# Performance work log

Hardware: AMD Instinct MI355X
Metric: run time of the kernel (lower is better)

The kernel has to match this reference:

```python
import jax, jax.numpy as jnp
import numpy as np

B = 8
C = 128          # channels
H = 1024         # sparse (hidden) channels in bottleneck
START = 128      # start_frames
SPARSE = 8192    # sparse_frames
K = 512          # k_sparse
N_UP = 6         # log2(SPARSE/START) upsample blocks
EPS = 1e-5


def conv1d(x, w, b, stride=1, pad=0):
    # x: (B, Cin, L), w: (Cout, Cin, K)
    y = jax.lax.conv_general_dilated(
        x, w, window_strides=(stride,), padding=[(pad, pad)],
        dimension_numbers=('NCW', 'OIW', 'NCW'))
    return y + b[None, :, None]


def batch_norm(x, g, beta):
    # training-mode BatchNorm1d: stats over (batch, length) per channel
    m = x.mean(axis=(0, 2), keepdims=True)
    v = x.var(axis=(0, 2), keepdims=True)
    return (x - m) * jax.lax.rsqrt(v + EPS) * g[None, :, None] + beta[None, :, None]


def lrelu(x):
    return jnp.where(x >= 0, x, 0.2 * x)


def setup_inputs() -> dict:
    key = jax.random.key(0)
    ks = jax.random.split(key, 16)
    s = 0.05
    return {
        'x': jax.random.normal(ks[0], (B, C, START), dtype=jnp.float32),
        'up_w': jax.random.normal(ks[1], (N_UP, C, C, 3), dtype=jnp.float32) * s,
        'up_b': jnp.zeros((N_UP, C), dtype=jnp.float32),
        'up_g': jnp.ones((N_UP, C), dtype=jnp.float32),
        'up_beta': jnp.zeros((N_UP, C), dtype=jnp.float32),
        'up_out_w': jax.random.normal(ks[2], (C, C, 3), dtype=jnp.float32) * s,
        'up_out_b': jnp.zeros((C,), dtype=jnp.float32),
        # SparseBottleneck 1x1 convs (stored as (out,in) matrices)
        'sb_up_w': jax.random.normal(ks[3], (H, C), dtype=jnp.float32) * s,
        'sb_up_b': jnp.zeros((H,), dtype=jnp.float32),
        'sal_w': jax.random.normal(ks[4], (H, C), dtype=jnp.float32) * s,
        'sal_b': jnp.zeros((H,), dtype=jnp.float32),
        'sb_down_w': jax.random.normal(ks[5], (C, H), dtype=jnp.float32) * s,
        'sb_down_b': jnp.zeros((C,), dtype=jnp.float32),
        'dn_w': jax.random.normal(ks[6], (3, C, C, 7), dtype=jnp.float32) * s,
        'dn_b': jnp.zeros((3, C), dtype=jnp.float32),
        'dn_g': jnp.ones((3, C), dtype=jnp.float32),
        'dn_beta': jnp.zeros((3, C), dtype=jnp.float32),
    }


def reference(x, up_w, up_b, up_g, up_beta, up_out_w, up_out_b,
              sb_up_w, sb_up_b, sal_w, sal_b, sb_down_w, sb_down_b,
              dn_w, dn_b, dn_g, dn_beta):
    # ---- ConvUpsample: 128 -> 8192 frames ----
    for i in range(N_UP):
        x = jnp.repeat(x, 2, axis=-1)
        x = conv1d(x, up_w[i], up_b[i], stride=1, pad=1)
        x = lrelu(batch_norm(x, up_g[i], up_beta[i]))
    x = conv1d(x, up_out_w, up_out_b, stride=1, pad=1)  # (B, C, 8192)

    # ---- SparseBottleneck ----
    sig = jnp.einsum('bcl,hc->bhl', x, sb_up_w) + sb_up_b[None, :, None]   # (B,H,L)
    sal = jnp.einsum('bcl,hc->bhl', x, sal_w) + sal_b[None, :, None]       # (B,H,L)
    flat = jax.nn.softmax(sal.reshape(B, -1), axis=-1)   # softmax over H*L
    vals, idx = jax.lax.top_k(flat, K)                   # (B, K)
    sparse = jnp.zeros_like(flat).at[jnp.arange(B)[:, None], idx].set(vals)
    sal = sparse.reshape(sal.shape)
    x = sig * sal                                         # gated, (B,H,L)
    x = jnp.einsum('bhl,ch->bcl', x, sb_down_w) + sb_down_b[None, :, None]

    # ---- down stack: 8192 -> 128 frames ----
    for i in range(3):
        x = conv1d(x, dn_w[i], dn_b[i], stride=4, pad=3)
        x = lrelu(x)
        x = batch_norm(x, dn_g[i], dn_beta[i])
    return x  # (B, C, 128)
```

## Files before the change

kernel.cpp:

```cpp
#include <hip/hip_runtime.h>
#include <hip/hip_bf16.h>


#define DEV_INLINE __device__ __forceinline__

constexpr int NB   = 8;
constexpr int NC   = 128;
constexpr int NH   = 1024;
constexpr int LFULL= 8192;
constexpr int KSEL = 512;
constexpr int CAP  = 32768;

typedef __attribute__((ext_vector_type(4))) float f32x4;
typedef __attribute__((ext_vector_type(8))) short bf16x8;

DEV_INLINE unsigned monoKey(float f) {
    unsigned u = __float_as_uint(f);
    return (u & 0x80000000u) ? ~u : (u | 0x80000000u);
}
DEV_INLINE float keyToF(unsigned k) {
    unsigned u = (k & 0x80000000u) ? (k ^ 0x80000000u) : ~k;
    return __uint_as_float(u);
}
DEV_INLINE unsigned monoKey16(unsigned u) {
    return (u & 0x8000u) ? ((~u) & 0xFFFFu) : (u | 0x8000u);
}
DEV_INLINE unsigned bf16r(float f) {
    unsigned u = __float_as_uint(f);
    return (u + 0x7FFFu + ((u >> 16) & 1u)) >> 16;
}
DEV_INLINE float lrelu(float v) { return v >= 0.f ? v : 0.2f * v; }
DEV_INLINE float f4c(const float4& v, int k) {
    return k == 0 ? v.x : k == 1 ? v.y : k == 2 ? v.z : v.w;
}
DEV_INLINE int swz4(int p) { return p ^ ((p >> 3) & 7); }

DEV_INLINE void loadg4(const float* __restrict__ rowp, int g0, int L, float* e) {
    if (g0 >= 0 && g0 + 4 <= L) {
        float4 v = *(const float4*)(rowp + g0);
        e[0] = v.x; e[1] = v.y; e[2] = v.z; e[3] = v.w;
    } else {
#pragma unroll
        for (int t = 0; t < 4; t++) {
            int g = g0 + t;
            e[t] = (g >= 0 && g < L) ? rowp[g] : 0.f;
        }
    }
}

__global__ __launch_bounds__(256) void prep_k(
    const float* __restrict__ up_w, const float* __restrict__ up_out_w,
    const float* __restrict__ dn_w, float* __restrict__ wprep)
{
    int idx = blockIdx.x * 256 + threadIdx.x;
    if (idx < 393216) {
        int layer = idx >> 16;
        int r0 = idx & 65535;
        int c = r0 >> 9, r = (r0 >> 7) & 3, o = r0 & 127;
        const float* wsrc = up_w + ((size_t)layer * 128 + o) * 384 + c * 3;
        float w0 = wsrc[0], w1 = wsrc[1], w2 = wsrc[2];
        wprep[idx] = (r == 0) ? w0 : (r == 1) ? (w1 + w2) : (r == 2) ? (w0 + w1) : w2;
    } else if (idx < 442368) {
        int r0 = idx - 393216;
        int c = r0 / 384, k = (r0 / 128) % 3, o = r0 & 127;
        wprep[idx] = up_out_w[((size_t)o * 128 + c) * 3 + k];
    } else {
        int r0 = idx - 442368;
        int layer = r0 / 114688;
        int r1 = r0 - layer * 114688;
        int c = r1 / 896, k = (r1 / 128) % 7, o = r1 & 127;
        wprep[idx] = dn_w[((size_t)layer * 128 + o) * 896 + c * 7 + k];
    }
}

__global__ __launch_bounds__(256) void prepA_k(
    const float* __restrict__ up_w, const float* __restrict__ up_out_w,
    unsigned short* __restrict__ afrag)
{
    int idx = blockIdx.x * 256 + threadIdx.x;
    if (idx >= 221184) return;
    int rid = idx >> 6, lane = idx & 63;
    const int r15 = lane & 15, g = lane >> 4;
    unsigned short vals[8];
    if (rid < 3072) {
        int L  = rid >> 9;
        int r0 = rid & 511;
        int f = r0 & 3, ks = (r0 >> 2) & 1, cc = (r0 >> 3) & 1;
        int wo = (r0 >> 4) & 1, half = (r0 >> 5) & 1, ptap = (r0 >> 6) & 3;
        int o = wo * 64 + f * 16 + r15;
        int cb = cc * 64 + ks * 32 + g * 8;
#pragma unroll
        for (int e = 0; e < 8; e++) {
            const float* ws = up_w + (((size_t)L * 128 + o) * 128 + (cb + e)) * 3;
            float w0 = ws[0], w1 = ws[1], w2 = ws[2];
            float v = (ptap == 0) ? w0 : (ptap == 1) ? (w1 + w2)
                    : (ptap == 2) ? (w0 + w1) : w2;
            unsigned hi = bf16r(v);
            if (half == 0) vals[e] = (unsigned short)hi;
            else vals[e] = (unsigned short)bf16r(v - __uint_as_float(hi << 16));
        }
    } else {
        int r2 = rid - 3072;
        int f = r2 & 3, ks = (r2 >> 2) & 1, cc = (r2 >> 3) & 1;
        int wo = (r2 >> 4) & 1, half = (r2 >> 5) & 1, tap = r2 >> 6;
        int o = wo * 64 + f * 16 + r15;
        int cb = cc * 64 + ks * 32 + g * 8;
#pragma unroll
        for (int e = 0; e < 8; e++) {
            float v = up_out_w[((size_t)o * 128 + (cb + e)) * 3 + tap];
            unsigned hi = bf16r(v);
            if (half == 0) vals[e] = (unsigned short)hi;
            else vals[e] = (unsigned short)bf16r(v - __uint_as_float(hi << 16));
        }
    }
    unsigned pk[4];
#pragma unroll
    for (int q = 0; q < 4; q++)
        pk[q] = (unsigned)vals[2*q] | ((unsigned)vals[2*q+1] << 16);
    *(uint4*)(afrag + (size_t)rid * 512 + lane * 8) = make_uint4(pk[0], pk[1], pk[2], pk[3]);
}

__global__ __launch_bounds__(256) void redstats_k(
    const float* __restrict__ partial, int nb, float* __restrict__ stats)
{
    const int c = threadIdx.x;
    float s0 = 0.f, s1 = 0.f, s2 = 0.f, s3 = 0.f;
    for (int i = blockIdx.x * 4; i < nb; i += gridDim.x * 4) {
        s0 += partial[(size_t)(i + 0) * 256 + c];
        s1 += partial[(size_t)(i + 1) * 256 + c];
        s2 += partial[(size_t)(i + 2) * 256 + c];
        s3 += partial[(size_t)(i + 3) * 256 + c];
    }
    float s = (s0 + s1) + (s2 + s3);
    if (s != 0.f || blockIdx.x == 0) atomicAdd(&stats[c], s);
}

template<int INMODE>
__global__ __launch_bounds__(512) void mconvU_k(
    const float* __restrict__ in, float* __restrict__ out,
    const unsigned short* __restrict__ afrag, const float* __restrict__ bias,
    const float* __restrict__ stp, const float* __restrict__ gp,
    const float* __restrict__ btp, float inv_n,
    float* __restrict__ partial, int L_in)
{
    __shared__ unsigned short Xh[66 * 64], Xl[66 * 64];
    __shared__ float scs[NC], shs[NC];
    __shared__ float sstat[256];

    const int b = blockIdx.y, tile0 = blockIdx.x * 64, tid = threadIdx.x;
    const int lane = tid & 63, wid = tid >> 6;
    const int wo = wid >> 2, par = (wid >> 1) & 1, jh = wid & 1;
    const int r15 = lane & 15, g = lane >> 4;
    const int bid = b * gridDim.x + blockIdx.x;

    if (tid < 256) sstat[tid] = 0.f;
    if (INMODE > 0) {
        for (int c = tid; c < NC; c += 512) {
            float m  = stp[c] * inv_n;
            float va = stp[NC + c] * inv_n - m * m;
            float sc = gp[c] * rsqrtf(va + 1e-5f);
            scs[c] = sc;
            shs[c] = btp[c] - m * sc;
        }
    }

    f32x4 acc[4][2];
#pragma unroll
    for (int i = 0; i < 4; i++)
#pragma unroll
        for (int j = 0; j < 2; j++) acc[i][j] = (f32x4)(0.f);

    for (int cc = 0; cc < 2; cc++) {
        __syncthreads();
        {
            int r = tid & 63;
            int l = tile0 - 1 + r;
            for (int c0 = (tid >> 6); c0 < 64; c0 += 8) {
                int c = cc * 64 + c0;
                float v = 0.f;
                if (l >= 0 && l < L_in) {
                    v = in[((size_t)b * NC + c) * L_in + l];
                    if (INMODE > 0) v = lrelu(v * scs[c] + shs[c]);
                }
                unsigned hi = bf16r(v);
                unsigned lo = bf16r(v - __uint_as_float(hi << 16));
                unsigned bo = ((unsigned)(r * 128 + c0 * 2)) ^ (((unsigned)(r & 7)) << 4);
                *(unsigned short*)((char*)Xh + bo) = (unsigned short)hi;
                *(unsigned short*)((char*)Xl + bo) = (unsigned short)lo;
            }
            if (tid < 128) {
                int r2 = 64 + (tid >> 6);
                int l2 = tile0 - 1 + r2;
                int c0 = tid & 63;
                int c = cc * 64 + c0;
                float v = 0.f;
                if (l2 >= 0 && l2 < L_in) {
                    v = in[((size_t)b * NC + c) * L_in + l2];
                    if (INMODE > 0) v = lrelu(v * scs[c] + shs[c]);
                }
                unsigned hi = bf16r(v);
                unsigned lo = bf16r(v - __uint_as_float(hi << 16));
                unsigned bo = ((unsigned)(r2 * 128 + c0 * 2)) ^ (((unsigned)(r2 & 7)) << 4);
                *(unsigned short*)((char*)Xh + bo) = (unsigned short)hi;
                *(unsigned short*)((char*)Xl + bo) = (unsigned short)lo;
            }
        }
        __syncthreads();
#pragma unroll
        for (int pt = 0; pt < 2; pt++) {
            const int ptap = par * 2 + pt;
            const int roff = (ptap == 0) ? 0 : (ptap == 3) ? 2 : 1;
#pragma unroll
            for (int combo = 0; combo < 3; combo++) {
                const int ah = (combo == 2) ? 1 : 0;
                const unsigned short* Xs = (combo == 1) ? Xl : Xh;
                bf16x8 af[8];
#pragma unroll
                for (int ks = 0; ks < 2; ks++)
#pragma unroll
                    for (int f = 0; f < 4; f++) {
                        int rec = ((((ptap * 2 + ah) * 2 + wo) * 2 + cc) * 2 + ks) * 4 + f;
                        af[ks * 4 + f] = *(const bf16x8*)(afrag + (size_t)rec * 512 + lane * 8);
                    }
#pragma unroll
                for (int ks = 0; ks < 2; ks++) {
                    bf16x8 bf_[2];
#pragma unroll
                    for (int j = 0; j < 2; j++) {
                        int row = (jh * 2 + j) * 16 + r15 + roff;
                        unsigned bo = ((unsigned)(row * 128 + ks * 64 + g * 16))
                                    ^ (((unsigned)(row & 7)) << 4);
                        bf_[j] = *(const bf16x8*)((const char*)Xs + bo);
                    }
#pragma unroll
                    for (int i = 0; i < 4; i++)
#pragma unroll
                        for (int j = 0; j < 2; j++)
                            acc[i][j] = __builtin_amdgcn_mfma_f32_16x16x32_bf16(
                                af[ks * 4 + i], bf_[j], acc[i][j], 0, 0, 0);
                }
            }
        }
    }

    const int L_out = 2 * L_in;
#pragma unroll
    for (int i = 0; i < 4; i++) {
#pragma unroll
        for (int r = 0; r < 4; r++) {
            const int o = wo * 64 + i * 16 + g * 4 + r;
            const float bv = bias[o];
            float s1 = 0.f, s2 = 0.f;
#pragma unroll
            for (int j = 0; j < 2; j++) {
                float v = acc[i][j][r] + bv;
                int lout = 2 * (tile0 + (jh * 2 + j) * 16 + r15) + par;
                out[((size_t)b * NC + o) * L_out + lout] = v;
                s1 += v; s2 += v * v;
            }
#pragma unroll
            for (int m = 1; m < 16; m <<= 1) {
                s1 += __shfl_xor(s1, m);
                s2 += __shfl_xor(s2, m);
            }
            if (r15 == 0) {
                atomicAdd(&sstat[o], s1);
                atomicAdd(&sstat[NC + o], s2);
            }
        }
    }
    __syncthreads();
    if (tid < 256) partial[(size_t)bid * 256 + tid] = sstat[tid];
}

__global__ __launch_bounds__(512) void mconvF_k(
    const float* __restrict__ in, float* __restrict__ out,
    const unsigned short* __restrict__ afrag, const float* __restrict__ bias,
    const float* __restrict__ stp, const float* __restrict__ gp,
    const float* __restrict__ btp, float inv_n,
    unsigned short* __restrict__ xtout)
{
    __shared__ unsigned short Xh[130 * 64], Xl[130 * 64];
    __shared__ float scs[NC], shs[NC];

    const int b = blockIdx.y, l0 = blockIdx.x * 128, tid = threadIdx.x;
    const int lane = tid & 63, wid = tid >> 6;
    const int wo = wid >> 2, wl = (wid & 3) * 32;
    const int r15 = lane & 15, g = lane >> 4;

    for (int c = tid; c < NC; c += 512) {
        float m  = stp[c] * inv_n;
        float va = stp[NC + c] * inv_n - m * m;
        float sc = gp[c] * rsqrtf(va + 1e-5f);
        scs[c] = sc;
        shs[c] = btp[c] - m * sc;
    }

    f32x4 acc[4][2];
#pragma unroll
    for (int i = 0; i < 4; i++)
#pragma unroll
        for (int j = 0; j < 2; j++) acc[i][j] = (f32x4)(0.f);

    for (int cc = 0; cc < 2; cc++) {
        __syncthreads();
        {
            int r = tid & 127;
            int l = l0 - 1 + r;
            for (int c0 = (tid >> 7); c0 < 64; c0 += 4) {
                int c = cc * 64 + c0;
                float v = 0.f;
                if (l >= 0 && l < LFULL) {
                    v = in[((size_t)b * NC + c) * LFULL + l];
                    v = lrelu(v * scs[c] + shs[c]);
                }
                unsigned hi = bf16r(v);
                unsigned lo = bf16r(v - __uint_as_float(hi << 16));
                unsigned bo = ((unsigned)(r * 128 + c0 * 2)) ^ (((unsigned)(r & 7)) << 4);
                *(unsigned short*)((char*)Xh + bo) = (unsigned short)hi;
                *(unsigned short*)((char*)Xl + bo) = (unsigned short)lo;
            }
            if (tid < 128) {
                int r2 = 128 + (tid >> 6);
                int l2 = l0 - 1 + r2;
                int c0 = tid & 63;
                int c = cc * 64 + c0;
                float v = 0.f;
                if (l2 >= 0 && l2 < LFULL) {
                    v = in[((size_t)b * NC + c) * LFULL + l2];
                    v = lrelu(v * scs[c] + shs[c]);
                }
                unsigned hi = bf16r(v);
                unsigned lo = bf16r(v - __uint_as_float(hi << 16));
                unsigned bo = ((unsigned)(r2 * 128 + c0 * 2)) ^ (((unsigned)(r2 & 7)) << 4);
                *(unsigned short*)((char*)Xh + bo) = (unsigned short)hi;
                *(unsigned short*)((char*)Xl + bo) = (unsigned short)lo;
            }
        }
        __syncthreads();
#pragma unroll
        for (int tap = 0; tap < 3; tap++) {
#pragma unroll
            for (int combo = 0; combo < 3; combo++) {
                const int ah = (combo == 2) ? 1 : 0;
                const unsigned short* Xs = (combo == 1) ? Xl : Xh;
                bf16x8 af[8];
#pragma unroll
                for (int ks = 0; ks < 2; ks++)
#pragma unroll
                    for (int f = 0; f < 4; f++) {
                        int rec = 3072 + ((((tap * 2 + ah) * 2 + wo) * 2 + cc) * 2 + ks) * 4 + f;
                        af[ks * 4 + f] = *(const bf16x8*)(afrag + (size_t)rec * 512 + lane * 8);
                    }
#pragma unroll
                for (int ks = 0; ks < 2; ks++) {
                    bf16x8 bf_[2];
#pragma unroll
                    for (int j = 0; j < 2; j++) {
                        int row = wl + j * 16 + r15 + tap;
                        unsigned bo = ((unsigned)(row * 128 + ks * 64 + g * 16))
                                    ^ (((unsigned)(row & 7)) << 4);
                        bf_[j] = *(const bf16x8*)((const char*)Xs + bo);
                    }
#pragma unroll
                    for (int i = 0; i < 4; i++)
#pragma unroll
                        for (int j = 0; j < 2; j++)
                            acc[i][j] = __builtin_amdgcn_mfma_f32_16x16x32_bf16(
                                af[ks * 4 + i], bf_[j], acc[i][j], 0, 0, 0);
                }
            }
        }
    }

#pragma unroll
    for (int i = 0; i < 4; i++) {
#pragma unroll
        for (int r = 0; r < 4; r++) {
            const int o = wo * 64 + i * 16 + g * 4 + r;
            const float bv = bias[o];
#pragma unroll
            for (int j = 0; j < 2; j++) {
                float v = acc[i][j][r] + bv;
                int l = l0 + wl + j * 16 + r15;
                out[((size_t)b * NC + o) * LFULL + l] = v;
                xtout[((size_t)b * LFULL + l) * NC + o] = (unsigned short)bf16r(v);
            }
        }
    }
}

template<int KW, int STRIDE, int PAD, bool UPS, int INMODE, bool OUTACT, bool STATS, int TT, bool XPOSE, int OCW>
__global__ __launch_bounds__(256) void conv7_k(
    const float* __restrict__ in, float* __restrict__ out,
    const float* __restrict__ wp, const float* __restrict__ bias,
    const float* __restrict__ stp, const float* __restrict__ gp,
    const float* __restrict__ btp, float inv_n,
    float* __restrict__ stats, unsigned short* __restrict__ xtout,
    int L_in, int L_out)
{
    constexpr int CC    = (KW == 7) ? 8 : 16;
    constexpr int PT    = 64 * TT;
    constexpr int TTO   = UPS ? 2 * TT : TT;
    constexpr int NWR   = UPS ? 4 : KW;
    constexpr int OCB   = 4 * OCW;
    constexpr int SPAN  = UPS ? (PT + 2) : ((PT - 1) * STRIDE + KW);
    constexpr int NCH   = (SPAN + 3) / 4;
    constexpr int NCH8  = (NCH + 7) & ~7;
    constexpr int XROW  = 4 * NCH8 + 4;
    constexpr int NLD   = (CC * NCH + 255) / 256;
    constexpr int XSPAN = UPS ? (TT + 2) : ((TT - 1) * STRIDE + KW);
    constexpr int STEP  = UPS ? TT : TT * STRIDE;
    constexpr int NWQ   = CC * NWR * (OCB / 4);
    static_assert((STEP & 3) == 0, "conv7 swizzle path requires STEP%4==0");
    static_assert(OCW == 4 || OCW == 8, "OCW must be 4 or 8");

    __shared__ float xs[CC][XROW];
    __shared__ float wls[CC * NWR * OCB];
    __shared__ float scs[NC], shs[NC];

    const int b = blockIdx.z, ocb = blockIdx.y, tid = threadIdx.x;
    const int t0 = blockIdx.x * PT, lane = tid & 63;
    const int wid = tid >> 6;
    const int oc0 = ocb * OCB + wid * OCW;
    const int gb = UPS ? (t0 - 1) : (t0 * STRIDE - PAD);

    if (INMODE > 0) {
        for (int c = tid; c < NC; c += 256) {
            float m  = stp[c] * inv_n;
            float va = stp[NC + c] * inv_n - m * m;
            float sc = gp[c] * rsqrtf(va + 1e-5f);
            scs[c] = sc;
            shs[c] = btp[c] - m * sc;
        }
        __syncthreads();
    }

    float acc[OCW][TTO];
#pragma unroll
    for (int i = 0; i < OCW; i++)
#pragma unroll
        for (int j = 0; j < TTO; j++) acc[i][j] = 0.f;

    float pre[NLD][4];

#define C7_STAGEW(CCBASE) do {                                              \
    for (int _u = tid; _u < NWQ; _u += 256) {                               \
        int _row = _u / (OCB / 4), _g8 = _u % (OCB / 4);                    \
        int _cl = _row / NWR, _t = _row % NWR;                              \
        ((float4*)wls)[_u] = *(const float4*)(wp +                          \
            ((size_t)((CCBASE) + _cl) * NWR + _t) * 128 + ocb * OCB + _g8 * 4); \
    }                                                                       \
} while (0)

#define C7_COMPCI(CI) do {                                                  \
    float _q[XSPAN];                                                        \
    const int _qb4 = lane * (STEP / 4);                                     \
    _Pragma("unroll")                                                       \
    for (int _u = 0; _u < XSPAN / 4; _u++) {                                \
        float4 _v = *(const float4*)&xs[CI][4 * swz4(_qb4 + _u)];           \
        _q[4*_u] = _v.x; _q[4*_u+1] = _v.y;                                 \
        _q[4*_u+2] = _v.z; _q[4*_u+3] = _v.w;                               \
    }                                                                       \
    if constexpr ((XSPAN & 3) != 0) {                                       \
        const int _pt = swz4(_qb4 + XSPAN / 4);                             \
        if constexpr ((XSPAN & 3) >= 2) {                                   \
            float2 _v = *(const float2*)&xs[CI][4 * _pt];                   \
            _q[(XSPAN & ~3)] = _v.x; _q[(XSPAN & ~3) + 1] = _v.y;           \
        }                                                                   \
        if constexpr ((XSPAN & 3) == 1)                                     \
            _q[XSPAN - 1] = xs[CI][4 * _pt];                                \
        else if constexpr ((XSPAN & 3) == 3)                                \
            _q[XSPAN - 1] = xs[CI][4 * _pt + 2];                            \
    }                                                                       \
    {                                                                       \
        _Pragma("unroll")                                                   \
        for (int _k = 0; _k < KW; _k++) {                                   \
            if constexpr (OCW == 8) {                                       \
                const float4 _w0 = *(const float4*)&wls[((CI) * NWR + _k) * OCB + wid * 8];     \
                const float4 _w1 = *(const float4*)&wls[((CI) * NWR + _k) * OCB + wid * 8 + 4]; \
                _Pragma("unroll")                                           \
                for (int _i = 0; _i < 8; _i++) {                            \
                    float _wv = f4c(_i < 4 ? _w0 : _w1, _i & 3);            \
                    _Pragma("unroll")                                       \
                    for (int _j = 0; _j < TT; _j++)                         \
                        acc[_i][_j] = fmaf(_wv, _q[_j * STRIDE + _k], acc[_i][_j]); \
                }                                                           \
            } else {                                                        \
                const float4 _w0 = *(const float4*)&wls[((CI) * NWR + _k) * OCB + wid * 4];     \
                _Pragma("unroll")                                           \
                for (int _i = 0; _i < 4; _i++) {                            \
                    float _wv = f4c(_w0, _i);                               \
                    _Pragma("unroll")                                       \
                    for (int _j = 0; _j < TT; _j++)                         \
                        acc[_i][_j] = fmaf(_wv, _q[_j * STRIDE + _k], acc[_i][_j]); \
                }                                                           \
            }                                                               \
        }                                                                   \
    }                                                                       \
} while (0)

#pragma unroll
    for (int u = 0; u < NLD; u++) {
        int idx = tid + u * 256;
        if (idx < CC * NCH) {
            int cl = idx / NCH, q = idx - cl * NCH;
            loadg4(in + ((size_t)b * NC + cl) * L_in, gb + 4 * q, L_in, pre[u]);
        }
    }
#pragma unroll
    for (int u = 0; u < NLD; u++) {
        int idx = tid + u * 256;
        if (idx < CC * NCH) {
            int cl = idx / NCH, q = idx - cl * NCH;
            int g0 = gb + 4 * q;
            float e[4];
#pragma unroll
            for (int t = 0; t < 4; t++) {
                float v = pre[u][t];
                if (INMODE > 0) {
                    int gg = g0 + t;
                    if (gg >= 0 && gg < L_in) {
                        float s = v * scs[cl] + shs[cl];
                        v = (INMODE == 2) ? lrelu(s) : s;
                    }
                }
                e[t] = v;
            }
            *(float4*)&xs[cl][4 * swz4(q)] = make_float4(e[0], e[1], e[2], e[3]);
        }
    }
    C7_STAGEW(0);
    __syncthreads();

    for (int cc = 0; cc < NC; cc += CC) {
        if (cc + CC < NC) {
#pragma unroll
            for (int u = 0; u < NLD; u++) {
                int idx = tid + u * 256;
                if (idx < CC * NCH) {
                    int cl = idx / NCH, q = idx - cl * NCH;
                    loadg4(in + ((size_t)b * NC + cc + CC + cl) * L_in,
                           gb + 4 * q, L_in, pre[u]);
                }
            }
        }
#pragma unroll
        for (int ci = 0; ci < CC; ci++) {
            C7_COMPCI(ci);
        }
        __syncthreads();
        if (cc + CC < NC) {
#pragma unroll
            for (int u = 0; u < NLD; u++) {
                int idx = tid + u * 256;
                if (idx < CC * NCH) {
                    int cl = idx / NCH, q = idx - cl * NCH;
                    int g0 = gb + 4 * q;
                    int c = cc + CC + cl;
                    float e[4];
#pragma unroll
                    for (int t = 0; t < 4; t++) {
                        float v = pre[u][t];
                        if (INMODE > 0) {
                            int gg = g0 + t;
                            if (gg >= 0 && gg < L_in) {
                                float s = v * scs[c] + shs[c];
                                v = (INMODE == 2) ? lrelu(s) : s;
                            }
                        }
                        e[t] = v;
                    }
                    *(float4*)&xs[cl][4 * swz4(q)] = make_float4(e[0], e[1], e[2], e[3]);
                }
            }
            C7_STAGEW(cc + CC);
            __syncthreads();
        }
    }
#undef C7_STAGEW
#undef C7_COMPCI

    const int po = t0 + lane * TTO;
#pragma unroll
    for (int i = 0; i < OCW; i++) {
        const int o = oc0 + i;
        const float bv = bias[o];
        float s1 = 0.f, s2 = 0.f;
        float tmpm[TTO];
#pragma unroll
        for (int j = 0; j < TTO; j++) {
            float v = acc[i][j] + bv;
            if (OUTACT) v = lrelu(v);
            tmpm[j] = v;
            if (STATS) { s1 += v; s2 += v * v; }
        }
        float* orow = out + ((size_t)b * NC + o) * L_out + po;
        if constexpr (TTO == 4)
            *(float4*)orow = make_float4(tmpm[0], tmpm[1], tmpm[2], tmpm[3]);
        else if constexpr (TTO == 2)
            *(float2*)orow = make_float2(tmpm[0], tmpm[1]);
        else
            orow[0] = tmpm[0];
        if (STATS) {
#pragma unroll
            for (int m = 1; m < 64; m <<= 1) {
                s1 += __shfl_xor(s1, m);
                s2 += __shfl_xor(s2, m);
            }
            if (lane == 0) {
                atomicAdd(&stats[o], s1);
                atomicAdd(&stats[NC + o], s2);
            }
        }
    }
}

__global__ __launch_bounds__(256) void cvtW_k(const float* __restrict__ W,
                                              unsigned short* __restrict__ Wbf)
{
    int i = blockIdx.x * 256 + threadIdx.x;
    const float4 a = *(const float4*)&W[i * 8];
    const float4 b = *(const float4*)&W[i * 8 + 4];
    unsigned pk[4];
    pk[0] = bf16r(a.x) | (bf16r(a.y) << 16);
    pk[1] = bf16r(a.z) | (bf16r(a.w) << 16);
    pk[2] = bf16r(b.x) | (bf16r(b.y) << 16);
    pk[3] = bf16r(b.z) | (bf16r(b.w) << 16);
    *(uint4*)&Wbf[i * 8] = make_uint4(pk[0], pk[1], pk[2], pk[3]);
}

template<int PHASE>
__global__ __launch_bounds__(256) void salM2_k(
    const unsigned short* __restrict__ xT, const unsigned short* __restrict__ Wbf,
    const float* __restrict__ bias, float* __restrict__ gsum,
    unsigned* __restrict__ ghist, const unsigned* __restrict__ thrv,
    unsigned* __restrict__ candcnt, unsigned* __restrict__ candI)
{
    __shared__ unsigned short Als[128 * 128];
    __shared__ unsigned short Bls[128 * 128];

    const int b  = blockIdx.z;
    const int h0 = blockIdx.y * 128;
    const int l0 = blockIdx.x * 128;
    const int tid = threadIdx.x;
    const int lane = tid & 63;
    const int wid = tid >> 6;
    const int wh = (wid >> 1) * 64;
    const int wl = (wid & 1) * 64;

    {
        const uint4* gA = (const uint4*)(Wbf + (size_t)h0 * NC);
        const uint4* gB = (const uint4*)(xT + ((size_t)b * LFULL + l0) * NC);
        char* cA = (char*)Als; char* cB = (char*)Bls;
        for (int i = tid; i < 2048; i += 256) {
            int row = i >> 4, q = i & 15;
            unsigned sw = (unsigned)(row * 256 + q * 16) ^ (((unsigned)(row & 7)) << 4);
            *(uint4*)(cA + sw) = gA[i];
        }
        for (int i = tid; i < 2048; i += 256) {
            int row = i >> 4, q = i & 15;
            unsigned sw = (unsigned)(row * 256 + q * 16) ^ (((unsigned)(row & 7)) << 4);
            *(uint4*)(cB + sw) = gB[i];
        }
    }
    __syncthreads();

    f32x4 acc[4][4];
#pragma unroll
    for (int i = 0; i < 4; i++)
#pragma unroll
        for (int j = 0; j < 4; j++) acc[i][j] = (f32x4)(0.f);

    const int r15 = lane & 15, g = lane >> 4;
#pragma unroll
    for (int ks = 0; ks < 4; ks++) {
        bf16x8 af[4], bfv[4];
#pragma unroll
        for (int f = 0; f < 4; f++) {
            int rowA = wh + f * 16 + r15;
            unsigned offA = (unsigned)(rowA * 256 + ks * 64 + g * 16)
                          ^ (((unsigned)(rowA & 7)) << 4);
            af[f] = *(const bf16x8*)((const char*)Als + offA);
            int rowB = wl + f * 16 + r15;
            unsigned offB = (unsigned)(rowB * 256 + ks * 64 + g * 16)
                          ^ (((unsigned)(rowB & 7)) << 4);
            bfv[f] = *(const bf16x8*)((const char*)Bls + offB);
        }
#pragma unroll
        for (int i = 0; i < 4; i++)
#pragma unroll
            for (int j = 0; j < 4; j++)
                acc[i][j] = __builtin_amdgcn_mfma_f32_16x16x32_bf16(
                    af[i], bfv[j], acc[i][j], 0, 0, 0);
    }

    if constexpr (PHASE == 0) {
        __syncthreads();
        unsigned* lhist = (unsigned*)Als;
        for (int i = tid; i < 8192; i += 256) lhist[i] = 0;
        __syncthreads();
        unsigned* myh = lhist + (tid & 1) * 4096;
        float expsum = 0.f;
#pragma unroll
        for (int i = 0; i < 4; i++) {
#pragma unroll
            for (int r = 0; r < 4; r++) {
                const int h = h0 + wh + i * 16 + g * 4 + r;
                const float bv = bias[h];
#pragma unroll
                for (int j = 0; j < 4; j++) {
                    float v = acc[i][j][r] + bv;
                    expsum += expf(v);
                    atomicAdd(&myh[monoKey16(bf16r(v)) >> 4], 1u);
                }
            }
        }
#pragma unroll
        for (int m = 1; m < 64; m <<= 1) expsum += __shfl_xor(expsum, m);
        float* red = (float*)Bls;
        if (lane == 0) red[wid] = expsum;
        __syncthreads();
        for (int i = tid; i < 4096; i += 256) {
            unsigned s = lhist[i] + lhist[4096 + i];
            if (s) atomicAdd(&ghist[b * 4096 + i], s);
        }
        if (tid == 0) atomicAdd(&gsum[b], red[0] + red[1] + red[2] + red[3]);
    } else {
        const unsigned thr = thrv[b * 2];
#pragma unroll
        for (int i = 0; i < 4; i++) {
#pragma unroll
            for (int r = 0; r < 4; r++) {
                const int h = h0 + wh + i * 16 + g * 4 + r;
                const float bv = bias[h];
#pragma unroll
                for (int j = 0; j < 4; j++) {
                    float v = acc[i][j][r] + bv;
                    bool pr = monoKey16(bf16r(v)) >= thr;
                    unsigned long long m = __ballot(pr);
                    if (m) {
                        int leader = __ffsll((unsigned long long)m) - 1;
                        int cnt = __popcll(m);
                        unsigned basepos = 0;
                        if (lane == leader)
                            basepos = atomicAdd(&candcnt[b], (unsigned)cnt);
                        basepos = __shfl(basepos, leader);
                        if (pr) {
                            int rr = __popcll(m & ((1ull << lane) - 1ull));
                            unsigned pos = basepos + (unsigned)rr;
                            if (pos < CAP) {
                                int l = l0 + wl + j * 16 + r15;
                                candI[b * CAP + pos] = (unsigned)((h << 13) | l);
                            }
                        }
                    }
                }
            }
        }
    }
}

__global__ __launch_bounds__(256) void scan2_k(
    const unsigned* __restrict__ ghist, unsigned* __restrict__ thrv)
{
    const int b = blockIdx.x, tid = threadIdx.x;
    __shared__ unsigned part[256];
    unsigned s = 0;
#pragma unroll
    for (int i = 0; i < 16; i++) s += ghist[b * 4096 + tid * 16 + i];
    part[tid] = s;
    __syncthreads();
    if (tid == 0) {
        unsigned cum = 0; int ch;
        for (ch = 255; ch >= 0; ch--) {
            if (cum + part[ch] >= KSEL) break;
            cum += part[ch];
        }
        int bin = 0;
        if (ch >= 0) {
            for (bin = ch * 16 + 15; bin > ch * 16; bin--) {
                unsigned c = ghist[b * 4096 + bin];
                if (cum + c >= KSEL) break;
                cum += c;
            }
        }
        int bcol = bin > 0 ? bin - 1 : 0;
        thrv[b * 2] = (unsigned)bcol << 4;
    }
}

__global__ __launch_bounds__(128) void recompute_k(
    const unsigned* __restrict__ candcnt, const unsigned* __restrict__ candI,
    const float* __restrict__ xu, const float* __restrict__ W,
    const float* __restrict__ bias, unsigned* __restrict__ candK)
{
    const int b = blockIdx.y;
    const unsigned cnt = min(candcnt[b], (unsigned)CAP);
    const int t = threadIdx.x;
    __shared__ float wsum[2];
    for (unsigned k = blockIdx.x; k < cnt; k += 1024) {
        unsigned e = candI[b * CAP + k];
        int h = e >> 13, l = e & 8191;
        float prod = W[h * NC + t] * xu[(b * NC + t) * LFULL + l];
#pragma unroll
        for (int m = 1; m < 64; m <<= 1) prod += __shfl_xor(prod, m);
        if ((t & 63) == 0) wsum[t >> 6] = prod;
        __syncthreads();
        if (t == 0) candK[b * CAP + k] = monoKey(wsum[0] + wsum[1] + bias[h]);
        __syncthreads();
    }
}

__global__ __launch_bounds__(256) void select2_k(
    const unsigned* __restrict__ candcnt, const unsigned* __restrict__ candK,
    const unsigned* __restrict__ candI,
    uint2* __restrict__ selected, unsigned* __restrict__ selcnt)
{
    const int b = blockIdx.x, tid = threadIdx.x;
    __shared__ unsigned h1[4096];
    __shared__ unsigned l2k[2048], l2i[2048];
    __shared__ unsigned part[256];
    __shared__ unsigned sh[8];

    const unsigned Nc = min(candcnt[b], (unsigned)CAP);
    const unsigned* kk = candK + b * CAP;
    const unsigned* ii = candI + b * CAP;
    uint2* sel = selected + b * KSEL;

    for (int i = tid; i < 4096; i += 256) h1[i] = 0;
    if (tid < 8) sh[tid] = 0;
    __syncthreads();
    for (unsigned i = tid; i < Nc; i += 256) atomicAdd(&h1[kk[i] >> 20], 1u);
    __syncthreads();
    {
        unsigned s = 0;
#pragma unroll
        for (int i = 0; i < 16; i++) s += h1[tid * 16 + i];
        part[tid] = s;
        __syncthreads();
        if (tid == 0) {
            unsigned cum = 0; int ch;
            for (ch = 255; ch >= 0; ch--) { if (cum + part[ch] >= KSEL) break; cum += part[ch]; }
            int bin = 0;
            if (ch >= 0)
                for (bin = ch * 16 + 15; bin > ch * 16; bin--) {
                    unsigned c = h1[bin];
                    if (cum + c >= KSEL) break;
                    cum += c;
                }
            sh[2] = (unsigned)bin; sh[3] = KSEL - cum;
        }
    }
    __syncthreads();
    const unsigned b1 = sh[2], need1 = sh[3];
    for (int i = tid; i < 1024; i += 256) h1[i] = 0;
    __syncthreads();
    for (unsigned i = tid; i < Nc; i += 256) {
        unsigned k = kk[i], bin = k >> 20;
        if (bin > b1) {
            unsigned p = atomicAdd(&sh[0], 1u);
            if (p < KSEL) sel[p] = make_uint2(k, ii[i]);
        } else if (bin == b1) {
            atomicAdd(&h1[(k >> 10) & 1023], 1u);
        }
    }
    __syncthreads();
    {
        unsigned s = 0;
#pragma unroll
        for (int i = 0; i < 4; i++) s += h1[tid * 4 + i];
        part[tid] = s;
        __syncthreads();
        if (tid == 0) {
            unsigned cum = 0; int ch;
            for (ch = 255; ch >= 0; ch--) { if (cum + part[ch] >= need1) break; cum += part[ch]; }
            int bin = 0;
            if (ch >= 0)
                for (bin = ch * 4 + 3; bin > ch * 4; bin--) {
                    unsigned c = h1[bin];
                    if (cum + c >= need1) break;
                    cum += c;
                }
            sh[4] = (unsigned)bin; sh[5] = need1 - cum;
        }
    }
    __syncthreads();
    const unsigned b2 = sh[4], need2 = sh[5];
    for (int i = tid; i < 1024; i += 256) h1[i] = 0;
    __syncthreads();
    for (unsigned i = tid; i < Nc; i += 256) {
        unsigned k = kk[i];
        if ((k >> 20) != b1) continue;
        unsigned mb = (k >> 10) & 1023;
        if (mb > b2) {
            unsigned p = atomicAdd(&sh[0], 1u);
            if (p < KSEL) sel[p] = make_uint2(k, ii[i]);
        } else if (mb == b2) {
            unsigned j = atomicAdd(&sh[1], 1u);
            if (j < 2048) { l2k[j] = k; l2i[j] = ii[i]; atomicAdd(&h1[k & 1023], 1u); }
        }
    }
    __syncthreads();
    const unsigned m2 = min(sh[1], 2048u);
    {
        unsigned s = 0;
#pragma unroll
        for (int i = 0; i < 4; i++) s += h1[tid * 4 + i];
        part[tid] = s;
        __syncthreads();
        if (tid == 0) {
            unsigned cum = 0; int ch;
            for (ch = 255; ch >= 0; ch--) { if (cum + part[ch] >= need2) break; cum += part[ch]; }
            int bin = 0;
            if (ch >= 0)
                for (bin = ch * 4 + 3; bin > ch * 4; bin--) {
                    unsigned c = h1[bin];
                    if (cum + c >= need2) break;
                    cum += c;
                }
            sh[6] = (unsigned)bin; sh[7] = need2 - cum;
        }
    }
    __syncthreads();
    const unsigned b3 = sh[6], need3 = sh[7];
    if (tid == 0) sh[1] = 0;
    __syncthreads();
    for (unsigned i = tid; i < m2; i += 256) {
        unsigned k = l2k[i], lb = k & 1023;
        if (lb > b3) {
            unsigned p = atomicAdd(&sh[0], 1u);
            if (p < KSEL) sel[p] = make_uint2(k, l2i[i]);
        } else if (lb == b3) {
            unsigned t = atomicAdd(&sh[1], 1u);
            if (t < need3) {
                unsigned p = atomicAdd(&sh[0], 1u);
                if (p < KSEL) sel[p] = make_uint2(k, l2i[i]);
            }
        }
    }
    __syncthreads();
    if (tid == 0) selcnt[b] = min(sh[0], (unsigned)KSEL);
}

__global__ void inity_k(float* __restrict__ y, const float* __restrict__ bias)
{
    int i = blockIdx.x * 256 + threadIdx.x;
    float bv = bias[(i >> 11) & 127];
    ((float4*)y)[i] = make_float4(bv, bv, bv, bv);
}

__global__ __launch_bounds__(128) void scatter_k(
    const uint2* __restrict__ selected, const unsigned* __restrict__ selcnt,
    const float* __restrict__ gsum, const float* __restrict__ xu,
    const float* __restrict__ upw, const float* __restrict__ upb,
    const float* __restrict__ dww, float* __restrict__ y)
{
    const int b = blockIdx.y, kidx = blockIdx.x;
    if (kidx >= (int)selcnt[b]) return;
    const uint2 s = selected[b * KSEL + kidx];
    const float salv = keyToF(s.x);
    const unsigned idx = s.y;
    const int h = idx >> 13, l = idx & 8191;
    const int t = threadIdx.x;

    float prod = upw[h * NC + t] * xu[(b * NC + t) * LFULL + l];
#pragma unroll
    for (int m = 1; m < 64; m <<= 1) prod += __shfl_xor(prod, m);
    __shared__ float wsum[2];
    if ((t & 63) == 0) wsum[t >> 6] = prod;
    __syncthreads();
    const float sig = wsum[0] + wsum[1] + upb[h];
    const float val = expf(salv) / gsum[b];
    const float g = sig * val;
    atomicAdd(&y[(b * NC + t) * LFULL + l], dww[t * NH + h] * g);
}

__global__ void apply_k(const float* __restrict__ in, const float* __restrict__ stats,
                        const float* __restrict__ g, const float* __restrict__ bt,
                        float* __restrict__ out, float inv_n)
{
    int i = blockIdx.x * 256 + threadIdx.x;
    int c = (i >> 7) & 127;
    float m  = stats[c] * inv_n;
    float va = stats[NC + c] * inv_n - m * m;
    float sc = g[c] * rsqrtf(va + 1e-5f);
    out[i] = in[i] * sc + (bt[c] - m * sc);
}

extern "C" void kernel_launch(void* const* d_in, const int* in_sizes, int n_in,
                              void* d_out, int out_size, void* d_ws, size_t ws_size,
                              hipStream_t stream)
{
    const float* x        = (const float*)d_in[0];
    const float* up_w     = (const float*)d_in[1];
    const float* up_b     = (const float*)d_in[2];
    const float* up_g     = (const float*)d_in[3];
    const float* up_beta  = (const float*)d_in[4];
    const float* up_out_w = (const float*)d_in[5];
    const float* up_out_b = (const float*)d_in[6];
    const float* sb_up_w  = (const float*)d_in[7];
    const float* sb_up_b  = (const float*)d_in[8];
    const float* sal_w    = (const float*)d_in[9];
    const float* sal_b    = (const float*)d_in[10];
    const float* sb_dn_w  = (const float*)d_in[11];
    const float* sb_dn_b  = (const float*)d_in[12];
    const float* dn_w     = (const float*)d_in[13];
    const float* dn_b     = (const float*)d_in[14];
    const float* dn_g     = (const float*)d_in[15];
    const float* dn_beta  = (const float*)d_in[16];

    char* ws = (char*)d_ws;
    float*          stats    = (float*)(ws + 0);
    float*          gsum     = (float*)(ws + 16384);
    unsigned*       thrv     = (unsigned*)(ws + 16416);
    unsigned*       candcnt  = (unsigned*)(ws + 16480);
    unsigned*       selcnt   = (unsigned*)(ws + 16512);
    uint2*          selected = (uint2*)(ws + 16640);
    unsigned*       ghist    = (unsigned*)(ws + 49408);
    unsigned*       candK    = (unsigned*)(ws + 180480);
    unsigned*       candI    = (unsigned*)(ws + 1229056);
    unsigned short* Wbf      = (unsigned short*)(ws + 2277632);
    float*          wprep    = (float*)(ws + 2539776);
    float*          B0       = (float*)(ws + 5685504);
    float*          B1       = (float*)(ws + 39239936);
    unsigned short* xT       = (unsigned short*)(ws + 72794368);
    float*          y        = (float*)(ws + 72794368);
    unsigned short* Afrag    = (unsigned short*)(ws + 117440512);
    float*          partial  = (float*)(ws + 121634816);

    hipMemsetAsync(d_ws, 0, 16544, stream);
    hipMemsetAsync(ws + 49408, 0, 131072, stream);

    cvtW_k<<<64,256,0,stream>>>(sal_w, Wbf);
    prep_k<<<3072,256,0,stream>>>(up_w, up_out_w, dn_w, wprep);
    prepA_k<<<864,256,0,stream>>>(up_w, up_out_w, Afrag);

    mconvU_k<0><<<dim3(2,NB),512,0,stream>>>(
        x, B0, Afrag, up_b, nullptr, nullptr, nullptr, 0.f, partial, 128);
    redstats_k<<<16,256,0,stream>>>(partial, 2*NB, stats);
    mconvU_k<2><<<dim3(4,NB),512,0,stream>>>(
        B0, B1, Afrag + 1*262144, up_b + NC,
        stats, up_g, up_beta, 1.f/(float)(NB*256), partial, 256);
    redstats_k<<<16,256,0,stream>>>(partial, 4*NB, stats + 256);
    mconvU_k<2><<<dim3(8,NB),512,0,stream>>>(
        B1, B0, Afrag + 2*262144, up_b + 2*NC,
        stats + 256, up_g + NC, up_beta + NC, 1.f/(float)(NB*512), partial, 512);
    redstats_k<<<16,256,0,stream>>>(partial, 8*NB, stats + 2*256);
    mconvU_k<2><<<dim3(16,NB),512,0,stream>>>(
        B0, B1, Afrag + 3*262144, up_b + 3*NC,
        stats + 2*256, up_g + 2*NC, up_beta + 2*NC, 1.f/(float)(NB*1024), partial, 1024);
    redstats_k<<<16,256,0,stream>>>(partial, 16*NB, stats + 3*256);
    mconvU_k<2><<<dim3(32,NB),512,0,stream>>>(
        B1, B0, Afrag + 4*262144, up_b + 4*NC,
        stats + 3*256, up_g + 3*NC, up_beta + 3*NC, 1.f/(float)(NB*2048), partial, 2048);
    redstats_k<<<16,256,0,stream>>>(partial, 32*NB, stats + 4*256);
    mconvU_k<2><<<dim3(64,NB),512,0,stream>>>(
        B0, B1, Afrag + 5*262144, up_b + 5*NC,
        stats + 4*256, up_g + 4*NC, up_beta + 4*NC, 1.f/(float)(NB*4096), partial, 4096);
    redstats_k<<<16,256,0,stream>>>(partial, 64*NB, stats + 5*256);
    mconvF_k<<<dim3(64,NB),512,0,stream>>>(
        B1, B0, Afrag, up_out_b,
        stats + 5*256, up_g + 5*NC, up_beta + 5*NC, 1.f/(float)(NB*LFULL), xT);

    salM2_k<0><<<dim3(64,8,NB),256,0,stream>>>(xT, Wbf, sal_b, gsum, ghist,
                                               nullptr, nullptr, nullptr);
    scan2_k<<<NB,256,0,stream>>>(ghist, thrv);
    salM2_k<1><<<dim3(64,8,NB),256,0,stream>>>(xT, Wbf, sal_b, nullptr, nullptr,
                                               thrv, candcnt, candI);
    recompute_k<<<dim3(1024,NB),128,0,stream>>>(candcnt, candI, B0, sal_w, sal_b, candK);
    select2_k<<<NB,256,0,stream>>>(candcnt, candK, candI, selected, selcnt);
    inity_k<<<(NB*NC*LFULL/4)/256,256,0,stream>>>(y, sb_dn_b);
    scatter_k<<<dim3(KSEL,NB),128,0,stream>>>(selected, selcnt, gsum, B0,
                                              sb_up_w, sb_up_b, sb_dn_w, y);

    conv7_k<7,4,3,false,0,true,true,2,false,4><<<dim3(16,8,NB),256,0,stream>>>(
        y, B1, wprep + 442368, dn_b, nullptr, nullptr, nullptr, 0.f,
        stats + 6*256, nullptr, 8192, 2048);
    conv7_k<7,4,3,false,1,true,true,1,false,4><<<dim3(8,8,NB),256,0,stream>>>(
        B1, B0, wprep + 442368 + 114688, dn_b + NC,
        stats + 6*256, dn_g, dn_beta, 1.f/(float)(NB*2048),
        stats + 7*256, nullptr, 2048, 512);
    conv7_k<7,4,3,false,1,true,true,1,false,4><<<dim3(2,8,NB),256,0,stream>>>(
        B0, B1, wprep + 442368 + 2*114688, dn_b + 2*NC,
        stats + 7*256, dn_g + NC, dn_beta + NC, 1.f/(float)(NB*512),
        stats + 8*256, nullptr, 512, 128);

    apply_k<<<(out_size + 255)/256,256,0,stream>>>(
        B1, stats + 8*256, dn_g + 2*NC, dn_beta + 2*NC, (float*)d_out,
        1.f/(float)(NB*128));
}
```

Baseline: 701.1 us.

## Replace dense first down-conv with constant-plus-sparse-correction using linearity

The bottleneck output is mostly the down-projection bias with at most 512 sparse nonzero positions per batch. Instead of materialising the full 8192-frame tensor and running the first stride-4 conv over it, the code computes the conv response to the constant bias analytically (with a left-edge variant for the padded first frame), fills the output with that constant, then adds per-selected-element corrections via atomics. A separate pass then applies LeakyReLU and accumulates BN stats. This removes a large dense write and conv over mostly-constant data, at the cost of atomic contention and care at the padded boundaries.

```diff
diff --git a/kernel.cpp b/kernel.cpp
--- a/kernel.cpp
+++ b/kernel.cpp
@@ -943,18 +943,11 @@
     if (tid == 0) selcnt[b] = min(sh[0], (unsigned)KSEL);
 }
 
-__global__ void inity_k(float* __restrict__ y, const float* __restrict__ bias)
-{
-    int i = blockIdx.x * 256 + threadIdx.x;
-    float bv = bias[(i >> 11) & 127];
-    ((float4*)y)[i] = make_float4(bv, bv, bv, bv);
-}
-
-__global__ __launch_bounds__(128) void scatter_k(
+__global__ __launch_bounds__(128) void scatter2_k(
     const uint2* __restrict__ selected, const unsigned* __restrict__ selcnt,
     const float* __restrict__ gsum, const float* __restrict__ xu,
     const float* __restrict__ upw, const float* __restrict__ upb,
-    const float* __restrict__ dww, float* __restrict__ y)
+    float* __restrict__ gval)
 {
     const int b = blockIdx.y, kidx = blockIdx.x;
     if (kidx >= (int)selcnt[b]) return;
@@ -970,10 +963,109 @@
     __shared__ float wsum[2];
     if ((t & 63) == 0) wsum[t >> 6] = prod;
     __syncthreads();
-    const float sig = wsum[0] + wsum[1] + upb[h];
-    const float val = expf(salv) / gsum[b];
-    const float g = sig * val;
-    atomicAdd(&y[(b * NC + t) * LFULL + l], dww[t * NH + h] * g);
+    if (t == 0) {
+        const float sig = wsum[0] + wsum[1] + upb[h];
+        gval[b * KSEL + kidx] = sig * (expf(salv) / gsum[b]);
+    }
+}
+
+__global__ __launch_bounds__(128) void dnconst_k(
+    const float* __restrict__ dn_w, const float* __restrict__ dnb,
+    const float* __restrict__ dn_b0, float* __restrict__ cst)
+{
+    const int o = threadIdx.x;
+    float accA = 0.f, accE = 0.f;
+    for (int c = 0; c < NC; c++) {
+        const float bv = dnb[c];
+        const float* wp = dn_w + ((size_t)o * NC + c) * 7;
+#pragma unroll
+        for (int k = 0; k < 7; k++) {
+            float w = wp[k];
+            accA += w * bv;
+            if (k >= 3) accE += w * bv;
+        }
+    }
+    cst[o]       = accA + dn_b0[o];
+    cst[NC + o]  = accE + dn_b0[o];
+}
+
+__global__ __launch_bounds__(256) void fillpre_k(
+    const float* __restrict__ cst, float* __restrict__ pre)
+{
+    const int row = blockIdx.x;
+    const int o = row & 127;
+    const float vI = cst[o], v0 = cst[NC + o];
+    float4* p = (float4*)(pre + (size_t)row * 2048);
+#pragma unroll
+    for (int u = 0; u < 2; u++) {
+        int q = threadIdx.x + u * 256;
+        float4 v = make_float4(vI, vI, vI, vI);
+        if (q == 0) v.x = v0;
+        p[q] = v;
+    }
+}
+
+__global__ __launch_bounds__(128) void corrdn_k(
+    const uint2* __restrict__ selected, const unsigned* __restrict__ selcnt,
+    const float* __restrict__ gval, const float* __restrict__ dww,
+    const float* __restrict__ w0p, float* __restrict__ pre)
+{
+    const int b = blockIdx.y, kidx = blockIdx.x;
+    if (kidx >= (int)selcnt[b]) return;
+    const unsigned idx = selected[b * KSEL + kidx].y;
+    const int h = idx >> 13, l = idx & 8191;
+    const float g = gval[b * KSEL + kidx];
+    const int o = threadIdx.x;
+
+    __shared__ float dlt[NC];
+    dlt[o] = dww[o * NH + h] * g;
+    __syncthreads();
+
+    const int tlo = (l <= 3) ? 0 : ((l - 3 + 3) >> 2);
+    const int thi = min(2047, (l + 3) >> 2);
+    for (int t = tlo; t <= thi; t++) {
+        const int k = l - 4 * t + 3;
+        float corr = 0.f;
+#pragma unroll 4
+        for (int c = 0; c < NC; c++)
+            corr += w0p[(size_t)c * 896 + k * 128 + o] * dlt[c];
+        atomicAdd(&pre[((size_t)b * NC + o) * 2048 + t], corr);
+    }
+}
+
+__global__ __launch_bounds__(256) void actstats_k(
+    float* __restrict__ pre, float* __restrict__ stats)
+{
+    const int row = blockIdx.x;
+    const int o = row & 127;
+    float4* p = (float4*)(pre + (size_t)row * 2048);
+    float s1 = 0.f, s2 = 0.f;
+#pragma unroll
+    for (int u = 0; u < 2; u++) {
+        int q = threadIdx.x + u * 256;
+        float4 v = p[q];
+        float e[4] = {v.x, v.y, v.z, v.w};
+#pragma unroll
+        for (int t = 0; t < 4; t++) {
+            float a = lrelu(e[t]);
+            e[t] = a;
+            s1 += a; s2 += a * a;
+        }
+        p[q] = make_float4(e[0], e[1], e[2], e[3]);
+    }
+#pragma unroll
+    for (int m = 1; m < 64; m <<= 1) {
+        s1 += __shfl_xor(s1, m);
+        s2 += __shfl_xor(s2, m);
+    }
+    __shared__ float red[8];
+    const int lane = threadIdx.x & 63, wid = threadIdx.x >> 6;
+    if (lane == 0) { red[wid] = s1; red[4 + wid] = s2; }
+    __syncthreads();
+    if (threadIdx.x == 0) {
+        atomicAdd(&stats[o],      red[0] + red[1] + red[2] + red[3]);
+        atomicAdd(&stats[NC + o], red[4] + red[5] + red[6] + red[7]);
+    }
 }
 
 __global__ void apply_k(const float* __restrict__ in, const float* __restrict__ stats,
@@ -1025,9 +1117,10 @@
     float*          B0       = (float*)(ws + 5685504);
     float*          B1       = (float*)(ws + 39239936);
     unsigned short* xT       = (unsigned short*)(ws + 72794368);
-    float*          y        = (float*)(ws + 72794368);
     unsigned short* Afrag    = (unsigned short*)(ws + 117440512);
     float*          partial  = (float*)(ws + 121634816);
+    float*          gval     = (float*)(ws + 122159104);
+    float*          cst      = (float*)(ws + 122175488);
 
     hipMemsetAsync(d_ws, 0, 16544, stream);
     hipMemsetAsync(ws + 49408, 0, 131072, stream);
@@ -1070,13 +1163,15 @@
                                                thrv, candcnt, candI);
     recompute_k<<<dim3(1024,NB),128,0,stream>>>(candcnt, candI, B0, sal_w, sal_b, candK);
     select2_k<<<NB,256,0,stream>>>(candcnt, candK, candI, selected, selcnt);
-    inity_k<<<(NB*NC*LFULL/4)/256,256,0,stream>>>(y, sb_dn_b);
-    scatter_k<<<dim3(KSEL,NB),128,0,stream>>>(selected, selcnt, gsum, B0,
-                                              sb_up_w, sb_up_b, sb_dn_w, y);
-
-    conv7_k<7,4,3,false,0,true,true,2,false,4><<<dim3(16,8,NB),256,0,stream>>>(
-        y, B1, wprep + 442368, dn_b, nullptr, nullptr, nullptr, 0.f,
-        stats + 6*256, nullptr, 8192, 2048);
+    scatter2_k<<<dim3(KSEL,NB),128,0,stream>>>(selected, selcnt, gsum, B0,
+                                               sb_up_w, sb_up_b, gval);
+
+    dnconst_k<<<1,128,0,stream>>>(dn_w, sb_dn_b, dn_b, cst);
+    fillpre_k<<<NB*NC,256,0,stream>>>(cst, B1);
+    corrdn_k<<<dim3(KSEL,NB),128,0,stream>>>(selected, selcnt, gval, sb_dn_w,
+                                             wprep + 442368, B1);
+    actstats_k<<<NB*NC,256,0,stream>>>(B1, stats + 6*256);
+
     conv7_k<7,4,3,false,1,true,true,1,false,4><<<dim3(8,8,NB),256,0,stream>>>(
         B1, B0, wprep + 442368 + 114688, dn_b + NC,
         stats + 6*256, dn_g, dn_beta, 1.f/(float)(NB*2048),
```

Measured after the change: 655.5 us. 6.5% less time.
